# Kernel tuning notes

Measured on AMD Instinct MI355X. Metric: run time of the kernel, lower is better.

## Reference

```python
import jax, jax.numpy as jnp
import numpy as np
from jax import lax

DIM = 64
DSTATE = 16
EXPAND = 2
DINNER = DIM * EXPAND
DTRANK = (DIM + 15) // 16  # ceil(d_model/16) = 4
B, D, H, W = 1, 24, 24, 24
EPS = 1e-5


def setup_inputs() -> dict:
    key = jax.random.key(0)
    ks = jax.random.split(key, 40)
    def nrm(i, shape, s=0.02):
        return jax.random.normal(ks[i], shape, jnp.float32) * s
    inp = {}
    inp['x'] = jax.random.normal(ks[0], (B, DIM, D, H, W), jnp.float32)
    # three directional view convs + instance-norm affine params
    inp['w1'] = nrm(1, (DIM, DIM, 3, 1, 1)); inp['b1'] = jnp.zeros((DIM,), jnp.float32)
    inp['g1'] = jnp.ones((DIM,), jnp.float32) + nrm(2, (DIM,)); inp['be1'] = nrm(3, (DIM,))
    inp['w2'] = nrm(4, (DIM, DIM, 1, 3, 1)); inp['b2'] = jnp.zeros((DIM,), jnp.float32)
    inp['g2'] = jnp.ones((DIM,), jnp.float32) + nrm(5, (DIM,)); inp['be2'] = nrm(6, (DIM,))
    inp['w3'] = nrm(7, (DIM, DIM, 1, 1, 3)); inp['b3'] = jnp.zeros((DIM,), jnp.float32)
    inp['g3'] = jnp.ones((DIM,), jnp.float32) + nrm(8, (DIM,)); inp['be3'] = nrm(9, (DIM,))
    # MambaUnit layernorm
    inp['ln_w'] = jnp.ones((DIM,), jnp.float32); inp['ln_b'] = jnp.zeros((DIM,), jnp.float32)
    # Mamba params (shared across the three views, as in the source)
    inp['in_proj_w'] = nrm(10, (2 * DINNER, DIM))
    inp['conv_w'] = jnp.ones((DINNER,), jnp.float32) + nrm(11, (DINNER,))  # d_conv=1 depthwise
    inp['conv_b'] = nrm(12, (DINNER,))
    inp['x_proj_w'] = nrm(13, (DTRANK + 2 * DSTATE, DINNER))
    inp['dt_w'] = nrm(14, (DINNER, DTRANK), 0.1)
    inp['dt_b'] = nrm(15, (DINNER,), 0.1)
    inp['A_log'] = jnp.log(jnp.tile(jnp.arange(1, DSTATE + 1, dtype=jnp.float32), (DINNER, 1)))
    inp['D_param'] = jnp.ones((DINNER,), jnp.float32)
    inp['out_proj_w'] = nrm(16, (DIM, DINNER))
    # fusion 1x1x1 conv + instance norm
    inp['wf'] = nrm(17, (DIM, 3 * DIM, 1, 1, 1)); inp['bf'] = jnp.zeros((DIM,), jnp.float32)
    inp['gf'] = jnp.ones((DIM,), jnp.float32) + nrm(18, (DIM,)); inp['bef'] = nrm(19, (DIM,))
    return inp


def silu(x):
    return x * jax.nn.sigmoid(x)


def conv3d(x, w, b, pad):
    out = lax.conv_general_dilated(
        x, w, (1, 1, 1), [(pad[0], pad[0]), (pad[1], pad[1]), (pad[2], pad[2])],
        dimension_numbers=('NCDHW', 'OIDHW', 'NCDHW'))
    return out + b[None, :, None, None, None]


def instance_norm(x, g, b):
    m = x.mean(axis=(2, 3, 4), keepdims=True)
    v = x.var(axis=(2, 3, 4), keepdims=True)  # biased, as in torch InstanceNorm
    return (x - m) / jnp.sqrt(v + EPS) * g[None, :, None, None, None] + b[None, :, None, None, None]


def layer_norm(x, g, b):
    m = x.mean(axis=-1, keepdims=True)
    v = x.var(axis=-1, keepdims=True)
    return (x - m) / jnp.sqrt(v + EPS) * g + b


def mamba(u, in_proj_w, conv_w, conv_b, x_proj_w, dt_w, dt_b, A_log, D_param, out_proj_w):
    # u: (B, L, d_model)
    xz = u @ in_proj_w.T                       # (B, L, 2*DINNER)
    xi, z = jnp.split(xz, 2, axis=-1)
    xi = silu(xi * conv_w + conv_b)            # d_conv=1 depthwise conv == per-channel affine
    xdbl = xi @ x_proj_w.T                     # (B, L, DTRANK + 2*DSTATE)
    dt = xdbl[..., :DTRANK]
    Bm = xdbl[..., DTRANK:DTRANK + DSTATE]
    Cm = xdbl[..., DTRANK + DSTATE:]
    dt = jax.nn.softplus(dt @ dt_w.T + dt_b)   # (B, L, DINNER)
    A = -jnp.exp(A_log)                        # (DINNER, DSTATE)
    dA = jnp.exp(dt[..., None] * A)            # (B, L, DINNER, DSTATE)
    dBx = dt[..., None] * Bm[:, :, None, :] * xi[..., None]
    def comb(c1, c2):
        a1, b1 = c1
        a2, b2 = c2
        return a1 * a2, a2 * b1 + b2
    _, h = lax.associative_scan(comb, (dA, dBx), axis=1)  # h: (B, L, DINNER, DSTATE)
    y = jnp.einsum('blin,bln->bli', h, Cm) + xi * D_param
    y = y * silu(z)
    return y @ out_proj_w.T


def mamba_unit(x5, ln_w, ln_b, mparams):
    Bb, C = x5.shape[:2]
    dims = x5.shape[2:]
    xf = jnp.transpose(x5.reshape(Bb, C, -1), (0, 2, 1))  # (B, L, C)
    xn = layer_norm(xf, ln_w, ln_b)
    y = mamba(xn, *mparams)
    return jnp.transpose(y, (0, 2, 1)).reshape(Bb, C, *dims)


def reference(x, w1, b1, g1, be1, w2, b2, g2, be2, w3, b3, g3, be3, ln_w, ln_b,
              in_proj_w, conv_w, conv_b, x_proj_w, dt_w, dt_b, A_log, D_param, out_proj_w,
              wf, bf, gf, bef):
    mparams = (in_proj_w, conv_w, conv_b, x_proj_w, dt_w, dt_b, A_log, D_param, out_proj_w)
    v1 = jax.nn.relu(instance_norm(conv3d(x, w1, b1, (1, 0, 0)), g1, be1))
    v2 = jax.nn.relu(instance_norm(conv3d(x, w2, b2, (0, 1, 0)), g2, be2))
    v3 = jax.nn.relu(instance_norm(conv3d(x, w3, b3, (0, 0, 1)), g3, be3))
    m1 = mamba_unit(v1, ln_w, ln_b, mparams)
    m2 = mamba_unit(v2, ln_w, ln_b, mparams)
    m3 = mamba_unit(v3, ln_w, ln_b, mparams)
    cat = jnp.concatenate([m1, m2, m3], axis=1)
    out = jax.nn.relu(instance_norm(conv3d(cat, wf, bf, (0, 0, 0)), gf, bef))
    return out
```

## Files before the change

### kernel.cpp

```cpp
#include <hip/hip_runtime.h>

#define LTOT 13824
#define NCH 108
#define CHL 128
#define EPSF 1e-5f

static const size_t OFF_U   = 1024;
static const size_t NU      = (size_t)3*LTOT*64;
static const size_t NXI     = (size_t)3*LTOT*128;
static const size_t NBM     = (size_t)3*LTOT*16;
static const size_t NAG     = (size_t)3*NCH*128*16;
static const size_t OFF_XIT = OFF_U   + NU;
static const size_t OFF_SZT = OFF_XIT + NXI;
static const size_t OFF_DTT = OFF_SZT + NXI;
static const size_t OFF_BMT = OFF_DTT + NXI;
static const size_t OFF_CMT = OFF_BMT + NBM;
static const size_t OFF_W2  = OFF_CMT + NBM;
static const size_t OFF_WT  = OFF_W2 + 24576;
static const size_t OFF_AGA = OFF_U;
static const size_t OFF_AGB = OFF_U + NAG;
static const size_t OFF_SEED= OFF_U + 2*NAG;
static const size_t OFF_FIN = OFF_DTT;

__device__ __forceinline__ float sigm(float x){ return 1.f/(1.f+__expf(-x)); }
__device__ __forceinline__ float siluf(float x){ return x*sigm(x); }
__device__ __forceinline__ float softplusf(float x){
    return fmaxf(x,0.f) + log1pf(__expf(-fabsf(x)));
}

template<int CTRL>
__device__ __forceinline__ float dpp_add(float x){
    int v = __builtin_amdgcn_update_dpp(0, __float_as_int(x), CTRL, 0xf, 0xf, true);
    return x + __int_as_float(v);
}
__device__ __forceinline__ float sum16(float x){
    x = dpp_add<0xB1>(x);
    x = dpp_add<0x4E>(x);
    x = dpp_add<0x141>(x);
    x = dpp_add<0x140>(x);
    return x;
}

__global__ __launch_bounds__(256) void k_wt(const float* __restrict__ w1,
                      const float* __restrict__ w2, const float* __restrict__ w3,
                      float* __restrict__ wt)
{
    int idx = blockIdx.x*256 + threadIdx.x;
    int r = idx / 12288, rem = idx % 12288;
    int k = rem >> 6, o = rem & 63;
    const float* W = (r==0)?w1:(r==1)?w2:w3;
    wt[idx] = W[o*192 + k];
}

__global__ __launch_bounds__(192) void k_conv(const float* __restrict__ x,
                       const float* __restrict__ wt,
                       const float* __restrict__ b1, const float* __restrict__ b2,
                       const float* __restrict__ b3,
                       float* __restrict__ u, float* __restrict__ ws)
{
    __shared__ __align__(16) float xs[64*3*24];
    __shared__ float wl[96*64];
    __shared__ float ssum[64], ssq[64];
    const int r = blockIdx.y;
    const int row = blockIdx.x;
    const int d = row/24, h = row%24;
    const float* Bz = (r==0)?b1:(r==1)?b2:b3;
    const int tid = threadIdx.x;

    for (int s = tid; s < 4608; s += 192){
        int w = s % 24; int kt = s / 24; int ic = kt/3, t = kt%3;
        int src = 0; bool valid = true;
        if (r==0){ int dd = d+t-1; valid = (dd>=0 && dd<24); src = (dd*24+h)*24 + w; }
        else if (r==1){ int hh = h+t-1; valid = (hh>=0 && hh<24); src = (d*24+hh)*24 + w; }
        else { int ww = w+t-1; valid = (ww>=0 && ww<24); src = row*24 + ww; }
        xs[s] = valid ? x[(size_t)ic*LTOT + src] : 0.f;
    }
    if (tid < 64){ ssum[tid]=0.f; ssq[tid]=0.f; }

    const int o = tid & 63, wg = tid >> 6, w0 = wg*8;
    float bias = Bz[o];
    float acc[8];
    #pragma unroll
    for (int j=0;j<8;j++) acc[j]=bias;

    const float* wtr = wt + (size_t)r*12288;
    for (int half=0; half<2; half++){
        __syncthreads();
        for (int s = tid; s < 6144; s += 192)
            wl[s] = wtr[half*6144 + s];
        __syncthreads();
        for (int ic2=0; ic2<32; ic2++){
            int ic = half*32 + ic2;
            #pragma unroll
            for (int t=0;t<3;t++){
                float wv = wl[(ic2*3+t)*64 + o];
                const float4* xp = (const float4*)&xs[(ic*3+t)*24 + w0];
                float4 a = xp[0], b = xp[1];
                acc[0]=fmaf(wv,a.x,acc[0]); acc[1]=fmaf(wv,a.y,acc[1]);
                acc[2]=fmaf(wv,a.z,acc[2]); acc[3]=fmaf(wv,a.w,acc[3]);
                acc[4]=fmaf(wv,b.x,acc[4]); acc[5]=fmaf(wv,b.y,acc[5]);
                acc[6]=fmaf(wv,b.z,acc[6]); acc[7]=fmaf(wv,b.w,acc[7]);
            }
        }
    }
    float ps=0.f, pq=0.f;
    size_t ub = ((size_t)r*LTOT + (size_t)row*24)*64;
    #pragma unroll
    for (int j=0;j<8;j++){
        float v = acc[j];
        u[ub + (size_t)(w0+j)*64 + o] = v;
        ps += v; pq += v*v;
    }
    atomicAdd(&ssum[o], ps); atomicAdd(&ssq[o], pq);
    __syncthreads();
    if (tid < 64){
        atomicAdd(&ws[r*64 + tid], ssum[tid]);
        atomicAdd(&ws[192 + r*64 + tid], ssq[tid]);
    }
}

__global__ __launch_bounds__(192) void k_stats1(float* ws){
    int t = threadIdx.x;
    float s = ws[t], q = ws[192+t];
    float m = s*(1.f/(float)LTOT);
    float v = q*(1.f/(float)LTOT) - m*m;
    ws[512+t] = m; ws[704+t] = rsqrtf(v + EPSF);
}

__global__ __launch_bounds__(256) void k_inproj(const float* __restrict__ u, float* __restrict__ xiT,
                         float* __restrict__ szT, const float* __restrict__ ipw,
                         const float* __restrict__ cw, const float* __restrict__ cb,
                         const float* __restrict__ ws,
                         const float* g1,const float* be1,const float* g2,const float* be2,
                         const float* g3,const float* be3,
                         const float* lnw,const float* lnb)
{
    __shared__ __align__(16) float xl[32*64];
    __shared__ float xo[32*257];
    const int tid = threadIdx.x, r = blockIdx.y;
    const int wv = tid >> 6, lane = tid & 63;
    const int l0 = blockIdx.x*32;
    size_t gbase = (size_t)r*LTOT + l0;

    float wr[64];
    const float4* wp = (const float4*)(ipw + (size_t)tid*64);
    #pragma unroll
    for (int q=0;q<16;q++){
        float4 u4 = wp[q];
        wr[4*q]=u4.x; wr[4*q+1]=u4.y; wr[4*q+2]=u4.z; wr[4*q+3]=u4.w;
    }

    {
        const float* g  = (r==0)?g1:(r==1)?g2:g3;
        const float* be = (r==0)?be1:(r==1)?be2:be3;
        float m  = ws[512 + r*64 + lane], rs = ws[704 + r*64 + lane];
        float gg = g[lane], bb = be[lane];
        float lw = lnw[lane], lb = lnb[lane];
        for (int j=0;j<8;j++){
            int p = 4*j + wv;
            float vv = u[(gbase+p)*64 + lane];
            vv = fmaxf((vv-m)*rs*gg + bb, 0.f);
            float s1 = sum16(vv), s2 = sum16(vv*vv);
            s1 += __shfl_xor(s1,16); s2 += __shfl_xor(s2,16);
            s1 += __shfl_xor(s1,32); s2 += __shfl_xor(s2,32);
            float mean = s1*(1.f/64.f);
            float var  = s2*(1.f/64.f) - mean*mean;
            xl[p*64 + lane] = (vv-mean)*rsqrtf(var+EPSF)*lw + lb;
        }
    }
    const bool isx = tid < 128;
    float ccw=0.f, ccb=0.f;
    if (isx){ ccw = cw[tid]; ccb = cb[tid]; }
    __syncthreads();

    #pragma unroll 4
    for (int p=0;p<32;p++){
        const float4* xp = (const float4*)&xl[p*64];
        float a0=0,a1=0,a2=0,a3=0;
        #pragma unroll
        for (int q=0;q<16;q++){
            float4 a = xp[q];
            a0=fmaf(wr[4*q],a.x,a0); a1=fmaf(wr[4*q+1],a.y,a1);
            a2=fmaf(wr[4*q+2],a.z,a2); a3=fmaf(wr[4*q+3],a.w,a3);
        }
        float acc = (a0+a1)+(a2+a3);
        float v = isx ? siluf(fmaf(acc, ccw, ccb)) : siluf(acc);
        xo[p*257 + tid] = v;
    }
    __syncthreads();

    for (int s = tid; s < 2048; s += 256){
        int ch = s >> 3, q = s & 7;
        float4 v = make_float4(xo[(q*4+0)*257+ch], xo[(q*4+1)*257+ch],
                               xo[(q*4+2)*257+ch], xo[(q*4+3)*257+ch]);
        float* dst = (ch < 128) ? xiT : szT;
        int c2 = ch & 127;
        *(float4*)&dst[((size_t)r*128 + c2)*LTOT + l0 + q*4] = v;
    }
}

__global__ __launch_bounds__(256) void k_xproj(const float* __restrict__ xiT, float* __restrict__ dtT,
                        float* __restrict__ BmT, float* __restrict__ CmT,
                        const float* __restrict__ xpw, const float* __restrict__ dtw,
                        const float* __restrict__ dtb)
{
    __shared__ __align__(16) float xt[128*36];
    __shared__ float ww[36*129];
    __shared__ float sd[4*36];
    const int tid = threadIdx.x, r = blockIdx.y;
    const int l0 = blockIdx.x*32;

    for (int s = tid; s < 4096; s += 256){
        int c = s>>5, p = s&31;
        xt[c*36+p] = xiT[((size_t)r*128 + c)*LTOT + l0 + p];
    }
    for (int s = tid; s < 4608; s += 256){
        int k = s>>7, c = s&127;
        ww[k*129+c] = xpw[s];
    }
    __syncthreads();

    const int wv = tid>>6, lane = tid&63;
    float acc[8] = {0,0,0,0,0,0,0,0};
    if (lane < 36){
        const float* wrow = &ww[lane*129];
        for (int c=0;c<128;c++){
            float w = wrow[c];
            float4 a = *(const float4*)&xt[c*36 + wv*8];
            float4 b = *(const float4*)&xt[c*36 + wv*8 + 4];
            acc[0]=fmaf(w,a.x,acc[0]); acc[1]=fmaf(w,a.y,acc[1]);
            acc[2]=fmaf(w,a.z,acc[2]); acc[3]=fmaf(w,a.w,acc[3]);
            acc[4]=fmaf(w,b.x,acc[4]); acc[5]=fmaf(w,b.y,acc[5]);
            acc[6]=fmaf(w,b.z,acc[6]); acc[7]=fmaf(w,b.w,acc[7]);
        }
    }
    if (lane>=4 && lane<36){
        float* dst = (lane<20) ? BmT : CmT;
        int n = (lane<20) ? (lane-4) : (lane-20);
        size_t base = ((size_t)r*16 + n)*LTOT + l0 + wv*8;
        *(float4*)&dst[base]   = make_float4(acc[0],acc[1],acc[2],acc[3]);
        *(float4*)&dst[base+4] = make_float4(acc[4],acc[5],acc[6],acc[7]);
    }
    if (lane < 4){
        #pragma unroll
        for (int p=0;p<8;p++) sd[lane*36 + wv*8 + p] = acc[p];
    }
    __syncthreads();

    const int i = tid>>1, ph = tid&1;
    float4 dw = *(const float4*)&dtw[i*4];
    float db = dtb[i];
    float buf[16];
    #pragma unroll
    for (int t=0;t<16;t++){
        int p = ph*16 + t;
        float v = db + dw.x*sd[0*36+p] + dw.y*sd[1*36+p]
                     + dw.z*sd[2*36+p] + dw.w*sd[3*36+p];
        buf[t] = softplusf(v);
    }
    size_t base = ((size_t)r*128 + i)*LTOT + l0 + ph*16;
    #pragma unroll
    for (int q=0;q<4;q++){
        *(float4*)&dtT[base + 4*q] =
            make_float4(buf[4*q], buf[4*q+1], buf[4*q+2], buf[4*q+3]);
    }
}

__global__ __launch_bounds__(256) void k_scan1(const float* __restrict__ dtT, const float* __restrict__ BmT,
                        const float* __restrict__ xiT, const float* __restrict__ Alog,
                        float* __restrict__ aga, float* __restrict__ agb)
{
    __shared__ float4 sdt[16*33], sxi[16*33], sbm[16*33];
    const int tid = threadIdx.x;
    const int n = tid & 15, il = tid >> 4;
    const int c = blockIdx.x, ib = blockIdx.y, r = blockIdx.z;
    const int i = ib*16 + il;

    for (int f = tid; f < 512; f += 256){
        int ii = f >> 5, t4 = f & 31;
        size_t rowI = ((size_t)r*128 + ib*16 + ii)*LTOT + (size_t)c*CHL + t4*4;
        size_t rowN = ((size_t)r*16  + ii)*LTOT + (size_t)c*CHL + t4*4;
        sdt[ii*33 + t4] = *(const float4*)&dtT[rowI];
        sxi[ii*33 + t4] = *(const float4*)&xiT[rowI];
        sbm[ii*33 + t4] = *(const float4*)&BmT[rowN];
    }
    __syncthreads();

    const float A2 = -expf(Alog[i*16+n]) * 1.44269504f;
    float b = 0.f, sdtacc = 0.f;
    #define S1_STEP(dv,xv,bv) { float e=exp2f(A2*(dv)); b=fmaf(e,b,(dv)*(xv)*(bv)); }
    for (int t4 = 0; t4 < 32; t4++){
        float4 d = sdt[il*33 + t4];
        float4 x = sxi[il*33 + t4];
        float4 m = sbm[n*33 + t4];
        sdtacc += ((d.x+d.y)+(d.z+d.w));
        S1_STEP(d.x,x.x,m.x) S1_STEP(d.y,x.y,m.y)
        S1_STEP(d.z,x.z,m.z) S1_STEP(d.w,x.w,m.w)
    }
    size_t o = ((size_t)(r*NCH+c)*128 + i)*16 + n;
    aga[o] = exp2f(A2*sdtacc);
    agb[o] = b;
}

__global__ __launch_bounds__(512) void k_scan2(const float* __restrict__ aga, const float* __restrict__ agb,
                        float* __restrict__ seed)
{
    int t = blockIdx.x*512 + threadIdx.x;
    int r = t >> 11, rem = t & 2047;
    float h = 0.f;
    for (int c=0;c<NCH;c++){
        size_t idx = (size_t)(r*NCH+c)*2048 + rem;
        float a = aga[idx], b = agb[idx];
        seed[idx] = h;
        h = fmaf(a, h, b);
    }
}

__global__ __launch_bounds__(256) void k_scan3(const float* __restrict__ dtT, const float* __restrict__ BmT,
                        const float* __restrict__ CmT, const float* __restrict__ xiT,
                        float* __restrict__ szT, const float* __restrict__ Alog,
                        const float* __restrict__ Dp, const float* __restrict__ seed)
{
    __shared__ float4 sdt[16*33], sxi[16*33], sbm[16*33], scm[16*33], ssz[16*33];
    const int tid = threadIdx.x;
    const int n = tid & 15, il = tid >> 4;
    const int c = blockIdx.x, ib = blockIdx.y, r = blockIdx.z;
    const int i = ib*16 + il;

    for (int f = tid; f < 512; f += 256){
        int ii = f >> 5, t4 = f & 31;
        size_t rowI = ((size_t)r*128 + ib*16 + ii)*LTOT + (size_t)c*CHL + t4*4;
        size_t rowN = ((size_t)r*16  + ii)*LTOT + (size_t)c*CHL + t4*4;
        sdt[ii*33 + t4] = *(const float4*)&dtT[rowI];
        sxi[ii*33 + t4] = *(const float4*)&xiT[rowI];
        ssz[ii*33 + t4] = *(const float4*)&szT[rowI];
        sbm[ii*33 + t4] = *(const float4*)&BmT[rowN];
        scm[ii*33 + t4] = *(const float4*)&CmT[rowN];
    }
    __syncthreads();

    const float A2 = -expf(Alog[i*16+n]) * 1.44269504f;
    const float Dv = Dp[i];
    float h = seed[(size_t)(r*NCH+c)*2048 + (i*16+n)];

    #define S3_STEP(dv,xv,bv,cv,oyv) { \
        float e=exp2f(A2*(dv)); h=fmaf(e,h,(dv)*(xv)*(bv)); \
        float py=sum16(h*(cv)); oyv = fmaf((xv),Dv,py); }
    for (int t4 = 0; t4 < 32; t4++){
        float4 d = sdt[il*33 + t4];
        float4 x = sxi[il*33 + t4];
        float4 m = sbm[n*33 + t4];
        float4 cv = scm[n*33 + t4];
        float4 yv;
        S3_STEP(d.x,x.x,m.x,cv.x, yv.x)
        S3_STEP(d.y,x.y,m.y,cv.y, yv.y)
        S3_STEP(d.z,x.z,m.z,cv.z, yv.z)
        S3_STEP(d.w,x.w,m.w,cv.w, yv.w)
        if (n==0){
            float4 s = ssz[il*33 + t4];
            ssz[il*33 + t4] = make_float4(yv.x*s.x, yv.y*s.y, yv.z*s.z, yv.w*s.w);
        }
    }
    __syncthreads();

    for (int f = tid; f < 512; f += 256){
        int ii = f >> 5, t4 = f & 31;
        size_t rowI = ((size_t)r*128 + ib*16 + ii)*LTOT + (size_t)c*CHL + t4*4;
        *(float4*)&szT[rowI] = ssz[ii*33 + t4];
    }
}

__global__ __launch_bounds__(256) void k_w2(const float* __restrict__ opw, const float* __restrict__ wf,
                     float* __restrict__ w2t)
{
    int idx = blockIdx.x*256 + threadIdx.x;
    int o = idx & 63, ri = idx >> 6;
    int r = ri >> 7, i = ri & 127;
    float acc = 0.f;
    for (int c2=0;c2<64;c2++)
        acc += opw[c2*128+i] * wf[o*192 + r*64 + c2];
    w2t[idx] = acc;
}

__global__ __launch_bounds__(256) void k_fin(const float* __restrict__ yT, const float* __restrict__ w2t,
                      const float* __restrict__ bfb, float* __restrict__ fin,
                      float* __restrict__ ws)
{
    __shared__ __align__(16) float yl[384*20];
    __shared__ float part[4*16*64];
    __shared__ float ssum[64], ssq[64];
    const int tid = threadIdx.x;
    const int l0 = blockIdx.x*16;
    const int o = tid & 63, sg = tid >> 6;

    for (int f = tid; f < 6144; f += 256){
        int k = f >> 4, p = f & 15;
        yl[k*20 + p] = yT[(size_t)k*LTOT + l0 + p];
    }
    float wreg[96];
    {
        const float* wp = w2t + (size_t)(sg*96)*64 + o;
        #pragma unroll
        for (int j=0;j<96;j++) wreg[j] = wp[(size_t)j*64];
    }
    if (tid < 64){ ssum[tid]=0.f; ssq[tid]=0.f; }
    __syncthreads();

    float acc[16];
    #pragma unroll
    for (int p=0;p<16;p++) acc[p]=0.f;
    #pragma unroll 4
    for (int j=0;j<96;j++){
        int k = sg*96 + j;
        float w = wreg[j];
        const float4* yp4 = (const float4*)&yl[k*20];
        float4 a = yp4[0], b = yp4[1], c = yp4[2], d = yp4[3];
        acc[0] =fmaf(w,a.x,acc[0]);  acc[1] =fmaf(w,a.y,acc[1]);
        acc[2] =fmaf(w,a.z,acc[2]);  acc[3] =fmaf(w,a.w,acc[3]);
        acc[4] =fmaf(w,b.x,acc[4]);  acc[5] =fmaf(w,b.y,acc[5]);
        acc[6] =fmaf(w,b.z,acc[6]);  acc[7] =fmaf(w,b.w,acc[7]);
        acc[8] =fmaf(w,c.x,acc[8]);  acc[9] =fmaf(w,c.y,acc[9]);
        acc[10]=fmaf(w,c.z,acc[10]); acc[11]=fmaf(w,c.w,acc[11]);
        acc[12]=fmaf(w,d.x,acc[12]); acc[13]=fmaf(w,d.y,acc[13]);
        acc[14]=fmaf(w,d.z,acc[14]); acc[15]=fmaf(w,d.w,acc[15]);
    }
    #pragma unroll
    for (int p=0;p<16;p++) part[(sg*16+p)*64 + o] = acc[p];
    __syncthreads();

    float bias = bfb[o];
    float ps=0.f, pq=0.f;
    #pragma unroll
    for (int j=0;j<4;j++){
        int p = sg + j*4;
        float s = part[(0*16+p)*64+o] + part[(1*16+p)*64+o]
                + part[(2*16+p)*64+o] + part[(3*16+p)*64+o] + bias;
        fin[(size_t)(l0+p)*64 + o] = s;
        ps += s; pq += s*s;
    }
    atomicAdd(&ssum[o], ps); atomicAdd(&ssq[o], pq);
    __syncthreads();
    if (tid<64){
        atomicAdd(&ws[384+tid], ssum[tid]);
        atomicAdd(&ws[448+tid], ssq[tid]);
    }
}

__global__ __launch_bounds__(64) void k_statsF(float* ws){
    int t = threadIdx.x;
    float s = ws[384+t], q = ws[448+t];
    float m = s*(1.f/(float)LTOT);
    float v = q*(1.f/(float)LTOT) - m*m;
    ws[896+t] = m; ws[960+t] = rsqrtf(v + EPSF);
}

__global__ __launch_bounds__(256) void k_out(const float* __restrict__ fin, const float* __restrict__ ws,
                      const float* __restrict__ gf, const float* __restrict__ bef,
                      float* __restrict__ out)
{
    __shared__ float tl[64*65];
    const int tid = threadIdx.x;
    const int l0 = blockIdx.x*64;
    for (int s=tid; s<4096; s+=256){
        int li = s>>6, o = s&63;
        float v = fin[(size_t)(l0+li)*64 + o];
        v = fmaxf((v - ws[896+o])*ws[960+o]*gf[o] + bef[o], 0.f);
        tl[o*65+li] = v;
    }
    __syncthreads();
    for (int s=tid; s<4096; s+=256){
        int o = s>>6, li = s&63;
        out[(size_t)o*LTOT + l0 + li] = tl[o*65+li];
    }
}

extern "C" void kernel_launch(void* const* d_in, const int* in_sizes, int n_in,
                              void* d_out, int out_size, void* d_ws, size_t ws_size,
                              hipStream_t stream)
{
    const float* X    = (const float*)d_in[0];
    const float* W1   = (const float*)d_in[1];  const float* B1  = (const float*)d_in[2];
    const float* G1   = (const float*)d_in[3];  const float* BE1 = (const float*)d_in[4];
    const float* W2   = (const float*)d_in[5];  const float* B2  = (const float*)d_in[6];
    const float* G2   = (const float*)d_in[7];  const float* BE2 = (const float*)d_in[8];
    const float* W3   = (const float*)d_in[9];  const float* B3  = (const float*)d_in[10];
    const float* G3   = (const float*)d_in[11]; const float* BE3 = (const float*)d_in[12];
    const float* LNW  = (const float*)d_in[13]; const float* LNB = (const float*)d_in[14];
    const float* IPW  = (const float*)d_in[15];
    const float* CW   = (const float*)d_in[16]; const float* CB  = (const float*)d_in[17];
    const float* XPW  = (const float*)d_in[18];
    const float* DTW  = (const float*)d_in[19]; const float* DTB = (const float*)d_in[20];
    const float* ALOG = (const float*)d_in[21]; const float* DP  = (const float*)d_in[22];
    const float* OPW  = (const float*)d_in[23];
    const float* WF   = (const float*)d_in[24]; const float* BF  = (const float*)d_in[25];
    const float* GF   = (const float*)d_in[26]; const float* BEF = (const float*)d_in[27];
    float* ws = (float*)d_ws;

    (void)hipMemsetAsync(d_ws, 0, 2048, stream);

    k_wt    <<<144, 256, 0, stream>>>(W1, W2, W3, ws+OFF_WT);
    k_conv  <<<dim3(576,3), 192, 0, stream>>>(X, ws+OFF_WT, B1, B2, B3, ws+OFF_U, ws);
    k_stats1<<<1, 192, 0, stream>>>(ws);
    k_inproj<<<dim3(432,3), 256, 0, stream>>>(ws+OFF_U, ws+OFF_XIT, ws+OFF_SZT,
                                              IPW, CW, CB, ws,
                                              G1,BE1,G2,BE2,G3,BE3, LNW,LNB);
    k_xproj <<<dim3(432,3), 256, 0, stream>>>(ws+OFF_XIT, ws+OFF_DTT, ws+OFF_BMT,
                                              ws+OFF_CMT, XPW, DTW, DTB);
    k_scan1 <<<dim3(NCH,8,3), 256, 0, stream>>>(ws+OFF_DTT, ws+OFF_BMT, ws+OFF_XIT,
                                                ALOG, ws+OFF_AGA, ws+OFF_AGB);
    k_scan2 <<<12, 512, 0, stream>>>(ws+OFF_AGA, ws+OFF_AGB, ws+OFF_SEED);
    k_scan3 <<<dim3(NCH,8,3), 256, 0, stream>>>(ws+OFF_DTT, ws+OFF_BMT, ws+OFF_CMT,
                                                ws+OFF_XIT, ws+OFF_SZT, ALOG, DP,
                                                ws+OFF_SEED);
    k_w2    <<<96, 256, 0, stream>>>(OPW, WF, ws+OFF_W2);
    k_fin   <<<864, 256, 0, stream>>>(ws+OFF_SZT, ws+OFF_W2, BF, ws+OFF_FIN, ws);
    k_statsF<<<1, 64, 0, stream>>>(ws);
    k_out   <<<216, 256, 0, stream>>>(ws+OFF_FIN, ws, GF, BEF, (float*)d_out);
}
```

Measured before the change: 437.2 us.

## Process two rows per conv block with 4x4 register tiles

The directional conv kernel now handles two spatial rows per block, so each staged weight tile is reused across twice as many outputs and half as many blocks reload weights. Each thread computes a 4-output-channel by 4-position tile using float4 shared-memory loads for both weights and inputs, which cuts shared-memory traffic per FMA. Output stores become float4. In exchange, shared memory per block grows and the grid halves, which may reduce occupancy and parallelism. The conv is only one of many kernels in the pipeline.

```diff
diff --git a/kernel.cpp b/kernel.cpp
--- a/kernel.cpp
+++ b/kernel.cpp
@@ -58,32 +58,40 @@
                        const float* __restrict__ b3,
                        float* __restrict__ u, float* __restrict__ ws)
 {
-    __shared__ __align__(16) float xs[64*3*24];
-    __shared__ float wl[96*64];
+    __shared__ __align__(16) float xs[2*4608];
+    __shared__ __align__(16) float wl[96*64];
     __shared__ float ssum[64], ssq[64];
     const int r = blockIdx.y;
-    const int row = blockIdx.x;
-    const int d = row/24, h = row%24;
+    const int row0 = blockIdx.x*2;
     const float* Bz = (r==0)?b1:(r==1)?b2:b3;
     const int tid = threadIdx.x;
 
-    for (int s = tid; s < 4608; s += 192){
-        int w = s % 24; int kt = s / 24; int ic = kt/3, t = kt%3;
-        int src = 0; bool valid = true;
-        if (r==0){ int dd = d+t-1; valid = (dd>=0 && dd<24); src = (dd*24+h)*24 + w; }
-        else if (r==1){ int hh = h+t-1; valid = (hh>=0 && hh<24); src = (d*24+hh)*24 + w; }
-        else { int ww = w+t-1; valid = (ww>=0 && ww<24); src = row*24 + ww; }
-        xs[s] = valid ? x[(size_t)ic*LTOT + src] : 0.f;
+    for (int rw2=0; rw2<2; rw2++){
+        int row = row0 + rw2;
+        int d = row/24, h = row%24;
+        for (int s = tid; s < 4608; s += 192){
+            int w = s % 24; int kt = s / 24; int ic = kt/3, t = kt%3;
+            int src = 0; bool valid = true;
+            if (r==0){ int dd = d+t-1; valid = (dd>=0 && dd<24); src = (dd*24+h)*24 + w; }
+            else if (r==1){ int hh = h+t-1; valid = (hh>=0 && hh<24); src = (d*24+hh)*24 + w; }
+            else { int ww = w+t-1; valid = (ww>=0 && ww<24); src = row*24 + ww; }
+            xs[rw2*4608 + s] = valid ? x[(size_t)ic*LTOT + src] : 0.f;
+        }
     }
     if (tid < 64){ ssum[tid]=0.f; ssq[tid]=0.f; }
 
-    const int o = tid & 63, wg = tid >> 6, w0 = wg*8;
-    float bias = Bz[o];
-    float acc[8];
-    #pragma unroll
-    for (int j=0;j<8;j++) acc[j]=bias;
+    const int rw = (tid >= 96) ? 1 : 0, t2 = tid - rw*96;
+    const int og = t2 & 15, wg2 = t2 >> 4;
+    const int o0 = og*4, w0 = wg2*4;
+    float acc[4][4];
+    {
+        float b0 = Bz[o0], b1v = Bz[o0+1], b2v = Bz[o0+2], b3v = Bz[o0+3];
+        #pragma unroll
+        for (int wj=0;wj<4;wj++){ acc[0][wj]=b0; acc[1][wj]=b1v; acc[2][wj]=b2v; acc[3][wj]=b3v; }
+    }
 
     const float* wtr = wt + (size_t)r*12288;
+    const float* xrow = &xs[rw*4608];
     for (int half=0; half<2; half++){
         __syncthreads();
         for (int s = tid; s < 6144; s += 192)
@@ -93,25 +101,34 @@
             int ic = half*32 + ic2;
             #pragma unroll
             for (int t=0;t<3;t++){
-                float wv = wl[(ic2*3+t)*64 + o];
-                const float4* xp = (const float4*)&xs[(ic*3+t)*24 + w0];
-                float4 a = xp[0], b = xp[1];
-                acc[0]=fmaf(wv,a.x,acc[0]); acc[1]=fmaf(wv,a.y,acc[1]);
-                acc[2]=fmaf(wv,a.z,acc[2]); acc[3]=fmaf(wv,a.w,acc[3]);
-                acc[4]=fmaf(wv,b.x,acc[4]); acc[5]=fmaf(wv,b.y,acc[5]);
-                acc[6]=fmaf(wv,b.z,acc[6]); acc[7]=fmaf(wv,b.w,acc[7]);
+                float4 wv = *(const float4*)&wl[(ic2*3+t)*64 + o0];
+                float4 xv = *(const float4*)&xrow[(ic*3+t)*24 + w0];
+                acc[0][0]=fmaf(wv.x,xv.x,acc[0][0]); acc[0][1]=fmaf(wv.x,xv.y,acc[0][1]);
+                acc[0][2]=fmaf(wv.x,xv.z,acc[0][2]); acc[0][3]=fmaf(wv.x,xv.w,acc[0][3]);
+                acc[1][0]=fmaf(wv.y,xv.x,acc[1][0]); acc[1][1]=fmaf(wv.y,xv.y,acc[1][1]);
+                acc[1][2]=fmaf(wv.y,xv.z,acc[1][2]); acc[1][3]=fmaf(wv.y,xv.w,acc[1][3]);
+                acc[2][0]=fmaf(wv.z,xv.x,acc[2][0]); acc[2][1]=fmaf(wv.z,xv.y,acc[2][1]);
+                acc[2][2]=fmaf(wv.z,xv.z,acc[2][2]); acc[2][3]=fmaf(wv.z,xv.w,acc[2][3]);
+                acc[3][0]=fmaf(wv.w,xv.x,acc[3][0]); acc[3][1]=fmaf(wv.w,xv.y,acc[3][1]);
+                acc[3][2]=fmaf(wv.w,xv.z,acc[3][2]); acc[3][3]=fmaf(wv.w,xv.w,acc[3][3]);
             }
         }
     }
-    float ps=0.f, pq=0.f;
-    size_t ub = ((size_t)r*LTOT + (size_t)row*24)*64;
-    #pragma unroll
-    for (int j=0;j<8;j++){
-        float v = acc[j];
-        u[ub + (size_t)(w0+j)*64 + o] = v;
-        ps += v; pq += v*v;
-    }
-    atomicAdd(&ssum[o], ps); atomicAdd(&ssq[o], pq);
+
+    size_t ub = ((size_t)r*LTOT + (size_t)(row0+rw)*24)*64;
+    float ps[4]={0,0,0,0}, pq[4]={0,0,0,0};
+    #pragma unroll
+    for (int wj=0; wj<4; wj++){
+        float4 v = make_float4(acc[0][wj],acc[1][wj],acc[2][wj],acc[3][wj]);
+        *(float4*)&u[ub + (size_t)(w0+wj)*64 + o0] = v;
+        ps[0]+=v.x; pq[0]+=v.x*v.x; ps[1]+=v.y; pq[1]+=v.y*v.y;
+        ps[2]+=v.z; pq[2]+=v.z*v.z; ps[3]+=v.w; pq[3]+=v.w*v.w;
+    }
+    #pragma unroll
+    for (int oj=0;oj<4;oj++){
+        atomicAdd(&ssum[o0+oj], ps[oj]);
+        atomicAdd(&ssq[o0+oj], pq[oj]);
+    }
     __syncthreads();
     if (tid < 64){
         atomicAdd(&ws[r*64 + tid], ssum[tid]);
@@ -499,7 +516,7 @@
     (void)hipMemsetAsync(d_ws, 0, 2048, stream);
 
     k_wt    <<<144, 256, 0, stream>>>(W1, W2, W3, ws+OFF_WT);
-    k_conv  <<<dim3(576,3), 192, 0, stream>>>(X, ws+OFF_WT, B1, B2, B3, ws+OFF_U, ws);
+    k_conv  <<<dim3(288,3), 192, 0, stream>>>(X, ws+OFF_WT, B1, B2, B3, ws+OFF_U, ws);
     k_stats1<<<1, 192, 0, stream>>>(ws);
     k_inproj<<<dim3(432,3), 256, 0, stream>>>(ws+OFF_U, ws+OFF_XIT, ws+OFF_SZT,
                                               IPW, CW, CB, ws,
```

New measurement: 435.0 us. No clear change (-0.5%).

## Restructure directional conv to position-per-lane with wave-uniform weights

Applied to the files above, without the earlier changes.

The directional 3-tap conv kernel is rewritten so each lane owns one spatial position and each wave computes 16 output channels. Input is read directly from global memory with coalesced loads, and weights become wave-uniform scalar loads instead of LDS-staged tiles. Instance-norm statistics now use wave reductions with per-channel global atomics instead of shared-memory atomics. Output is transposed through an LDS tile so stores are vectorized. This cuts LDS staging and block count, at the cost of more global input loads (each input value is read three times) and many atomics.

```diff
diff --git a/kernel.cpp b/kernel.cpp
--- a/kernel.cpp
+++ b/kernel.cpp
@@ -52,70 +52,71 @@
     wt[idx] = W[o*192 + k];
 }
 
-__global__ __launch_bounds__(192) void k_conv(const float* __restrict__ x,
+__global__ __launch_bounds__(256) void k_conv(const float* __restrict__ x,
                        const float* __restrict__ wt,
                        const float* __restrict__ b1, const float* __restrict__ b2,
                        const float* __restrict__ b3,
                        float* __restrict__ u, float* __restrict__ ws)
 {
-    __shared__ __align__(16) float xs[64*3*24];
-    __shared__ float wl[96*64];
-    __shared__ float ssum[64], ssq[64];
+    __shared__ float tl[64*65];
+    const int tid = threadIdx.x;
+    const int lane = tid & 63;
+    const int wv = __builtin_amdgcn_readfirstlane(tid >> 6);
     const int r = blockIdx.y;
-    const int row = blockIdx.x;
-    const int d = row/24, h = row%24;
-    const float* Bz = (r==0)?b1:(r==1)?b2:b3;
-    const int tid = threadIdx.x;
-
-    for (int s = tid; s < 4608; s += 192){
-        int w = s % 24; int kt = s / 24; int ic = kt/3, t = kt%3;
-        int src = 0; bool valid = true;
-        if (r==0){ int dd = d+t-1; valid = (dd>=0 && dd<24); src = (dd*24+h)*24 + w; }
-        else if (r==1){ int hh = h+t-1; valid = (hh>=0 && hh<24); src = (d*24+hh)*24 + w; }
-        else { int ww = w+t-1; valid = (ww>=0 && ww<24); src = row*24 + ww; }
-        xs[s] = valid ? x[(size_t)ic*LTOT + src] : 0.f;
-    }
-    if (tid < 64){ ssum[tid]=0.f; ssq[tid]=0.f; }
-
-    const int o = tid & 63, wg = tid >> 6, w0 = wg*8;
-    float bias = Bz[o];
-    float acc[8];
-    #pragma unroll
-    for (int j=0;j<8;j++) acc[j]=bias;
-
-    const float* wtr = wt + (size_t)r*12288;
-    for (int half=0; half<2; half++){
-        __syncthreads();
-        for (int s = tid; s < 6144; s += 192)
-            wl[s] = wtr[half*6144 + s];
-        __syncthreads();
-        for (int ic2=0; ic2<32; ic2++){
-            int ic = half*32 + ic2;
-            #pragma unroll
-            for (int t=0;t<3;t++){
-                float wv = wl[(ic2*3+t)*64 + o];
-                const float4* xp = (const float4*)&xs[(ic*3+t)*24 + w0];
-                float4 a = xp[0], b = xp[1];
-                acc[0]=fmaf(wv,a.x,acc[0]); acc[1]=fmaf(wv,a.y,acc[1]);
-                acc[2]=fmaf(wv,a.z,acc[2]); acc[3]=fmaf(wv,a.w,acc[3]);
-                acc[4]=fmaf(wv,b.x,acc[4]); acc[5]=fmaf(wv,b.y,acc[5]);
-                acc[6]=fmaf(wv,b.z,acc[6]); acc[7]=fmaf(wv,b.w,acc[7]);
-            }
+    const int p0 = blockIdx.x * 64;
+    const int pos = p0 + lane;
+    const int o0 = wv * 16;
+
+    const int wq = pos % 24, hq = (pos/24) % 24, dq = pos / 576;
+    const int co  = (r==0) ? dq : (r==1) ? hq : wq;
+    const bool vm = (co >= 1), vp = (co <= 22);
+    const int str = (r==0) ? 576 : (r==1) ? 24 : 1;
+
+    const float* xp  = x + pos;
+    const float* wtr = wt + (size_t)r*12288 + o0;
+    const float* Bz  = (r==0)?b1:(r==1)?b2:b3;
+
+    float acc[16];
+    #pragma unroll
+    for (int j=0;j<16;j++) acc[j] = 0.f;
+
+    for (int ic=0; ic<64; ic++){
+        const float* xc = xp + (size_t)ic*LTOT;
+        float xm = vm ? xc[-str] : 0.f;
+        float x0 = xc[0];
+        float xq = vp ? xc[str] : 0.f;
+        const float* wk = wtr + ic*192;
+        #pragma unroll
+        for (int j=0;j<16;j++){
+            float a = acc[j];
+            a = fmaf(wk[j],      xm, a);
+            a = fmaf(wk[64+j],   x0, a);
+            a = fmaf(wk[128+j],  xq, a);
+            acc[j] = a;
         }
     }
-    float ps=0.f, pq=0.f;
-    size_t ub = ((size_t)r*LTOT + (size_t)row*24)*64;
-    #pragma unroll
-    for (int j=0;j<8;j++){
+    #pragma unroll
+    for (int j=0;j<16;j++) acc[j] += Bz[o0+j];
+
+    #pragma unroll
+    for (int j=0;j<16;j++){
         float v = acc[j];
-        u[ub + (size_t)(w0+j)*64 + o] = v;
-        ps += v; pq += v*v;
-    }
-    atomicAdd(&ssum[o], ps); atomicAdd(&ssq[o], pq);
-    __syncthreads();
-    if (tid < 64){
-        atomicAdd(&ws[r*64 + tid], ssum[tid]);
-        atomicAdd(&ws[192 + r*64 + tid], ssq[tid]);
+        float s1 = sum16(v), s2 = sum16(v*v);
+        s1 += __shfl_xor(s1,16); s2 += __shfl_xor(s2,16);
+        s1 += __shfl_xor(s1,32); s2 += __shfl_xor(s2,32);
+        if (lane == j){
+            atomicAdd(&ws[r*64 + o0 + j], s1);
+            atomicAdd(&ws[192 + r*64 + o0 + j], s2);
+        }
+    }
+
+    #pragma unroll
+    for (int j=0;j<16;j++) tl[lane*65 + o0 + j] = acc[j];
+    __syncthreads();
+    for (int s = tid; s < 1024; s += 256){
+        int p = s >> 4, o = (s & 15) * 4;
+        float4 v = make_float4(tl[p*65+o], tl[p*65+o+1], tl[p*65+o+2], tl[p*65+o+3]);
+        *(float4*)&u[((size_t)r*LTOT + p0 + p)*64 + o] = v;
     }
 }
 
@@ -499,7 +500,7 @@
     (void)hipMemsetAsync(d_ws, 0, 2048, stream);
 
     k_wt    <<<144, 256, 0, stream>>>(W1, W2, W3, ws+OFF_WT);
-    k_conv  <<<dim3(576,3), 192, 0, stream>>>(X, ws+OFF_WT, B1, B2, B3, ws+OFF_U, ws);
+    k_conv  <<<dim3(216,3), 256, 0, stream>>>(X, ws+OFF_WT, B1, B2, B3, ws+OFF_U, ws);
     k_stats1<<<1, 192, 0, stream>>>(ws);
     k_inproj<<<dim3(432,3), 256, 0, stream>>>(ws+OFF_U, ws+OFF_XIT, ws+OFF_SZT,
                                               IPW, CW, CB, ws,
```

After: 478.7 us. 9.5% more time.
